# Optimization experiments

Measured on AMD Instinct MI355X. Metric: run time of the kernel, lower is better.

The kernel has to match this reference:

```python
import jax, jax.numpy as jnp
import numpy as np

NQ = 4  # n_qubits == hidden_dim, fixed by the hard-coded 4-wire encoder


def _cnot(state, c, t):
    # state: [B, 2,2,2,2]; wire w lives on axis w+1. Flip target where control==1.
    s = jnp.moveaxis(state, (c + 1, t + 1), (-2, -1))
    s = s.at[..., 1, :].set(s[..., 1, ::-1])
    return jnp.moveaxis(s, (-2, -1), (c + 1, t + 1))


def _qlayer(x, theta):
    """4-qubit circuit: RX(x_w) then RX(theta_w) on each wire (composed as one
    RX(x_w+theta_w) rotation, identical math), CNOT ring, PauliZ expectation.
    x: [B, 4] angles, theta: [4] trainable angles -> [B, 4] expectations."""
    half = (x + theta) * 0.5                      # [B,4]
    c = jnp.cos(half).astype(jnp.complex64)
    s = jnp.sin(half).astype(jnp.complex64)
    # RX(a)|0> = [cos(a/2), -i sin(a/2)]; product state of 4 qubits
    q = jnp.stack([c, -1j * s], axis=-1)          # [B,4,2]
    state = jnp.einsum('bi,bj,bk,bl->bijkl', q[:, 0], q[:, 1], q[:, 2], q[:, 3])
    # CNOT ring: (0,1), (1,2), (2,3), (3,0)
    state = _cnot(state, 0, 1)
    state = _cnot(state, 1, 2)
    state = _cnot(state, 2, 3)
    state = _cnot(state, 3, 0)
    p = jnp.real(state * jnp.conj(state))         # [B,2,2,2,2] probabilities
    sgn = jnp.asarray([1.0, -1.0], dtype=p.dtype)
    z0 = jnp.einsum('bijkl,i->b', p, sgn)
    z1 = jnp.einsum('bijkl,j->b', p, sgn)
    z2 = jnp.einsum('bijkl,k->b', p, sgn)
    z3 = jnp.einsum('bijkl,l->b', p, sgn)
    return jnp.stack([z0, z1, z2, z3], axis=-1)   # [B,4]


def setup_inputs() -> dict:
    key = jax.random.key(0)
    T, B, D, H = 512, 4096, 32, NQ
    ks = jax.random.split(key, 13)
    scale = 1.0 / np.sqrt(D + H)
    inp = {'inputs': jax.random.normal(ks[0], (T, B, D), dtype=jnp.float32)}
    names = ['f', 'i', 'u', 'o']
    for n, kw, kb, kt in zip(names, ks[1:5], ks[5:9], ks[9:13]):
        inp['W_' + n] = jax.random.uniform(kw, (D + H, NQ), jnp.float32, -scale, scale)
        inp['b_' + n] = jax.random.uniform(kb, (NQ,), jnp.float32, -scale, scale)
        inp['th_' + n] = jax.random.normal(kt, (NQ,), jnp.float32)
    return inp


def reference(inputs, W_f, b_f, W_i, b_i, W_u, b_u, W_o, b_o, th_f, th_i, th_u, th_o):
    B = inputs.shape[1]
    hx0 = jnp.zeros((B, NQ), dtype=inputs.dtype)
    cx0 = jnp.zeros((B, NQ), dtype=inputs.dtype)

    def step(carry, x):
        hx, cx = carry
        comb = jnp.concatenate([x, hx], axis=1)           # [B, D+H]
        f = jax.nn.sigmoid(_qlayer(comb @ W_f + b_f, th_f))
        i = jax.nn.sigmoid(_qlayer(comb @ W_i + b_i, th_i))
        g = jnp.tanh(_qlayer(comb @ W_u + b_u, th_u))
        o = jax.nn.sigmoid(_qlayer(comb @ W_o + b_o, th_o))
        cx2 = f * cx + i * g
        hx2 = o * jnp.tanh(cx2)
        return (hx2, cx2), hx2

    (hx, cx), outputs = jax.lax.scan(step, (hx0, cx0), inputs)
    return outputs, (hx, cx)
```

## Files before the change

### kernel.cpp

```cpp
#include <hip/hip_runtime.h>
#include <hip/hip_fp16.h>

#define TT 512
#define BB 4096
#define PD 16

__device__ __forceinline__ const float* sel4(int g, const float* a, const float* b,
                                             const float* c, const float* d) {
    return g == 0 ? a : (g == 1 ? b : (g == 2 ? c : d));
}

__device__ __forceinline__ float sigmoid_fast(float x) {
    float e = __expf(-x);
    return __builtin_amdgcn_rcpf(1.0f + e);
}
__device__ __forceinline__ float tanh_fast(float x) {
    float e = __expf(-2.0f * x);
    return fmaf(2.0f, __builtin_amdgcn_rcpf(1.0f + e), -1.0f);
}

template<int CTRL>
__device__ __forceinline__ float dppf(float v) {
    int i = __builtin_amdgcn_mov_dpp(__float_as_int(v), CTRL, 0xf, 0xf, true);
    return __int_as_float(i);
}
#define QP(a,b,c,d) ((a) | ((b) << 2) | ((c) << 4) | ((d) << 6))
template<int CTRL>
__device__ __forceinline__ float quad_bcast(float v) { return dppf<CTRL>(v); }

template<int OFS>
__device__ __forceinline__ float swzf(float v) {
    return __int_as_float(__builtin_amdgcn_ds_swizzle(__float_as_int(v), OFS));
}

__global__ __launch_bounds__(256) void qlstm_pre(
    const float* __restrict__ x,
    const float* __restrict__ Wf, const float* __restrict__ bf, const float* __restrict__ thf,
    const float* __restrict__ Wi, const float* __restrict__ bi, const float* __restrict__ thi,
    const float* __restrict__ Wu, const float* __restrict__ bu, const float* __restrict__ thu,
    const float* __restrict__ Wo, const float* __restrict__ bo, const float* __restrict__ tho,
    __half* __restrict__ Ax)
{
    __shared__ float4 Wl[32][4];
    __shared__ float4 bias4[4];
    __shared__ float xs[256 * 33];
    int tid = threadIdx.x;
    for (int idx = tid; idx < 512; idx += 256) {
        int j = idx >> 4, c = idx & 15, g = c >> 2, w = c & 3;
        ((float*)Wl)[idx] = sel4(g, Wf, Wi, Wu, Wo)[j * 4 + w];
    }
    if (tid < 16) {
        int g = tid >> 2, w = tid & 3;
        ((float*)bias4)[tid] = sel4(g, bf, bi, bu, bo)[w] + sel4(g, thf, thi, thu, tho)[w];
    }

    size_t rbase = (size_t)blockIdx.x * 256;
    const float4* xg = (const float4*)(x + rbase * 32);
#pragma unroll
    for (int it = 0; it < 8; ++it) {
        int i = it * 256 + tid;
        float4 v = xg[i];
        int r = i >> 3, c = (i & 7) * 4;
        float* p = &xs[r * 33 + c];
        p[0] = v.x; p[1] = v.y; p[2] = v.z; p[3] = v.w;
    }
    __syncthreads();

    float4 acc[4];
#pragma unroll
    for (int q = 0; q < 4; ++q) acc[q] = bias4[q];

    const float* xr = &xs[tid * 33];
#pragma unroll
    for (int j = 0; j < 32; ++j) {
        float xj = xr[j];
#pragma unroll
        for (int q = 0; q < 4; ++q) {
            float4 wv = Wl[j][q];
            acc[q].x = fmaf(xj, wv.x, acc[q].x);
            acc[q].y = fmaf(xj, wv.y, acc[q].y);
            acc[q].z = fmaf(xj, wv.z, acc[q].z);
            acc[q].w = fmaf(xj, wv.w, acc[q].w);
        }
    }

    union { __half2 h2; unsigned u; } cv;
    uint4 s0, s1;
    cv.h2 = __floats2half2_rn(acc[0].x, acc[0].y); s0.x = cv.u;
    cv.h2 = __floats2half2_rn(acc[0].z, acc[0].w); s0.y = cv.u;
    cv.h2 = __floats2half2_rn(acc[1].x, acc[1].y); s0.z = cv.u;
    cv.h2 = __floats2half2_rn(acc[1].z, acc[1].w); s0.w = cv.u;
    cv.h2 = __floats2half2_rn(acc[2].x, acc[2].y); s1.x = cv.u;
    cv.h2 = __floats2half2_rn(acc[2].z, acc[2].w); s1.y = cv.u;
    cv.h2 = __floats2half2_rn(acc[3].x, acc[3].y); s1.z = cv.u;
    cv.h2 = __floats2half2_rn(acc[3].z, acc[3].w); s1.w = cv.u;
    uint4* Ap = (uint4*)Ax + (rbase + tid) * 2;
    Ap[0] = s0; Ap[1] = s1;
}

__global__ __launch_bounds__(256) void qlstm_scan16(
    const __half* __restrict__ Ax,
    const float* __restrict__ Wf, const float* __restrict__ Wi,
    const float* __restrict__ Wu, const float* __restrict__ Wo,
    float* __restrict__ out)
{
    int tid = threadIdx.x;
    int gid = blockIdx.x * 256 + tid;
    int b   = gid >> 4;
    int L   = gid & 15;
    int w   = L & 3;
    int g   = L >> 2;

    const float* Wg = sel4(g, Wf, Wi, Wu, Wo);
    float whA = Wg[(32 + w) * 4 + w];
    float whB = Wg[(32 + (w ^ 1)) * 4 + w];
    float whC = Wg[(32 + (w ^ 2)) * 4 + w];
    float whD = Wg[(32 + (w ^ 3)) * 4 + w];
    bool isU = (g == 2);
    bool wb0 = (w & 1) != 0, wb1 = (w & 2) != 0;

    float d0 = isU ? 0.0f : 0.5f;
    float d1 = isU ? 1.0f : 0.25f;
    float d3 = isU ? -0.33333333f : -0.020833333f;
    float d5 = isU ? 0.13333333f : 0.0020833333f;
    float d7 = isU ? -0.03841007f : -0.000210846f;

    const __half* Axp = Ax + (size_t)b * 16 + L;
    float* outp4 = out + (size_t)b * 4 + L;

    float hx = 0.f, cx = 0.f;
    __half buf[PD];
#pragma unroll
    for (int k = 0; k < PD; ++k) buf[k] = Axp[(size_t)k * (BB * 16)];

#define SCAN_STEP(t, PREFETCH)                                                  \
    do {                                                                        \
        float ax = __half2float(buf[k]);                                        \
        if (PREFETCH) buf[k] = Axp[(size_t)((t) + PD) * (BB * 16)];             \
        float h1 = dppf<QP(1, 0, 3, 2)>(hx);                                    \
        float h2 = dppf<QP(2, 3, 0, 1)>(hx);                                    \
        float h3 = dppf<QP(3, 2, 1, 0)>(hx);                                    \
        float t1 = fmaf(hx, whA, ax);                                           \
        t1 = fmaf(h1, whB, t1);                                                 \
        float t2 = fmaf(h3, whD, h2 * whC);                                     \
        float C = __cosf(t1 + t2);                                              \
        float Cx1 = dppf<QP(1, 0, 3, 2)>(C);                                    \
        float P   = C * Cx1;                                                    \
        float Px2 = dppf<QP(2, 3, 0, 1)>(P);                                    \
        float Q   = P * Px2;                                                    \
        float m   = wb1 ? C : Cx1;                                              \
        float T   = Px2 * m;                                                    \
        float z   = wb0 ? (wb1 ? Q : P) : T;                                    \
        float z2  = z * z;                                                      \
        float pp  = fmaf(z2, d7, d5);                                           \
        pp = fmaf(z2, pp, d3);                                                  \
        pp = fmaf(z2, pp, d1);                                                  \
        float act = fmaf(z, pp, d0);                                            \
        float f = swzf<0x0013>(act);         \
        float i = swzf<0x0093>(act);                                \
        float u = swzf<0x0113>(act);                                \
        float o = swzf<0x0193>(act);                                \
        float c2 = fmaf(f, cx, i * u);                                          \
        cx = c2;                                                                \
        float q2 = c2 * c2;                                                     \
        float q4 = q2 * q2;                                                     \
        float dn = fmaf(q2, 420.0f, fmaf(q4, 15.0f, 945.0f));                   \
        float nm = c2 * fmaf(q2, 105.0f, 945.0f + q4);                          \
        hx = o * (nm * __builtin_amdgcn_rcpf(dn));                              \
        hxs[k] = hx;                                                            \
    } while (0)

    for (int tc = 0; tc < TT - PD; tc += PD) {
        float hxs[PD];
#pragma unroll
        for (int k = 0; k < PD; ++k) { int t = tc + k; SCAN_STEP(t, 1); }
        if (L < 4) {
#pragma unroll
            for (int k = 0; k < PD; ++k)
                outp4[(size_t)(tc + k) * 16384] = hxs[k];
        }
    }
    {
        float hxs[PD];
#pragma unroll
        for (int k = 0; k < PD; ++k) { int t = TT - PD + k; SCAN_STEP(t, 0); }
        if (L < 4) {
#pragma unroll
            for (int k = 0; k < PD; ++k)
                outp4[(size_t)(TT - PD + k) * 16384] = hxs[k];
        }
    }
    if (L < 4) {
        outp4[(size_t)TT * 16384] = hx;
        outp4[(size_t)TT * 16384 + 16384] = cx;
    }
#undef SCAN_STEP
}

__global__ __launch_bounds__(64, 1) void qlstm_scan_fb(
    const float* __restrict__ x,
    const float* __restrict__ Wf, const float* __restrict__ bf, const float* __restrict__ thf,
    const float* __restrict__ Wi, const float* __restrict__ bi, const float* __restrict__ thi,
    const float* __restrict__ Wu, const float* __restrict__ bu, const float* __restrict__ thu,
    const float* __restrict__ Wo, const float* __restrict__ bo, const float* __restrict__ tho,
    float* __restrict__ out)
{
    int lane = threadIdx.x;
    int gid  = blockIdx.x * 64 + lane;
    int b    = gid >> 2;
    int g    = lane & 3;

    const float* Wg = sel4(g, Wf, Wi, Wu, Wo);
    float wh[4][4];
#pragma unroll
    for (int j = 0; j < 4; ++j)
#pragma unroll
        for (int w = 0; w < 4; ++w)
            wh[j][w] = Wg[(32 + j) * 4 + w];

    __shared__ float4 Wl[32][4];
    float bias[4];
    for (int idx = lane; idx < 512; idx += 64) {
        int j = idx >> 4, c = idx & 15, gg = c >> 2, w = c & 3;
        ((float*)Wl)[idx] = sel4(gg, Wf, Wi, Wu, Wo)[j * 4 + w];
    }
#pragma unroll
    for (int w = 0; w < 4; ++w)
        bias[w] = sel4(g, bf, bi, bu, bo)[w] + sel4(g, thf, thi, thu, tho)[w];
    __syncthreads();

    float hx[4] = {0, 0, 0, 0}, cx[4] = {0, 0, 0, 0};
    const float4* xp = (const float4*)x + (size_t)b * 8;

    for (int t = 0; t < TT; ++t) {
        float4 xc[8];
#pragma unroll
        for (int k = 0; k < 8; ++k) xc[k] = xp[(size_t)t * (BB * 8) + k];
        float ax[4];
#pragma unroll
        for (int w = 0; w < 4; ++w) ax[w] = bias[w];
#pragma unroll
        for (int j = 0; j < 32; ++j) {
            float xj = ((const float*)xc)[j];
            float4 wv = Wl[j][g];
            ax[0] = fmaf(xj, wv.x, ax[0]);
            ax[1] = fmaf(xj, wv.y, ax[1]);
            ax[2] = fmaf(xj, wv.z, ax[2]);
            ax[3] = fmaf(xj, wv.w, ax[3]);
        }
        float C[4];
#pragma unroll
        for (int w = 0; w < 4; ++w) {
            float a0 = fmaf(hx[0], wh[0][w], ax[w]);
            float a1 = fmaf(hx[2], wh[2][w], hx[1] * wh[1][w]);
            a0 = fmaf(hx[3], wh[3][w], a0);
            C[w] = __cosf(a0 + a1);
        }
        float t12 = C[1] * C[2];
        float z[4];
        z[1] = C[0] * C[1];
        z[2] = C[0] * t12;
        z[0] = t12 * C[3];
        z[3] = z[2] * C[3];
        bool isU = (g == 2);
        float act[4];
#pragma unroll
        for (int w = 0; w < 4; ++w) {
            float zz = isU ? z[w] + z[w] : z[w];
            float y = sigmoid_fast(zz);
            act[w] = isU ? fmaf(2.0f, y, -1.0f) : y;
        }
#pragma unroll
        for (int w = 0; w < 4; ++w) {
            float fw = quad_bcast<QP(0, 0, 0, 0)>(act[w]);
            float iw = quad_bcast<QP(1, 1, 1, 1)>(act[w]);
            float uw = quad_bcast<QP(2, 2, 2, 2)>(act[w]);
            float ow = quad_bcast<QP(3, 3, 3, 3)>(act[w]);
            float c2 = fmaf(fw, cx[w], iw * uw);
            cx[w] = c2;
            hx[w] = ow * tanh_fast(c2);
        }
        float o01 = (g & 1) ? hx[1] : hx[0];
        float o23 = (g & 1) ? hx[3] : hx[2];
        out[(size_t)t * 16384 + gid] = (g & 2) ? o23 : o01;
    }
    float o01 = (g & 1) ? hx[1] : hx[0];
    float o23 = (g & 1) ? hx[3] : hx[2];
    out[(size_t)TT * 16384 + gid] = (g & 2) ? o23 : o01;
    float c01 = (g & 1) ? cx[1] : cx[0];
    float c23 = (g & 1) ? cx[3] : cx[2];
    out[(size_t)TT * 16384 + 16384 + gid] = (g & 2) ? c23 : c01;
}

extern "C" void kernel_launch(void* const* d_in, const int* in_sizes, int n_in,
                              void* d_out, int out_size, void* d_ws, size_t ws_size,
                              hipStream_t stream) {
    const float* x   = (const float*)d_in[0];
    const float* Wf  = (const float*)d_in[1];
    const float* bf  = (const float*)d_in[2];
    const float* thf = (const float*)d_in[3];
    const float* Wi  = (const float*)d_in[4];
    const float* bi  = (const float*)d_in[5];
    const float* thi = (const float*)d_in[6];
    const float* Wu  = (const float*)d_in[7];
    const float* bu  = (const float*)d_in[8];
    const float* thu = (const float*)d_in[9];
    const float* Wo  = (const float*)d_in[10];
    const float* bo  = (const float*)d_in[11];
    const float* tho = (const float*)d_in[12];
    float* out = (float*)d_out;

    size_t need = (size_t)TT * BB * 16 * sizeof(__half);
    if (ws_size >= need) {
        __half* Ax = (__half*)d_ws;
        qlstm_pre<<<(TT * BB) / 256, 256, 0, stream>>>(
            x, Wf, bf, thf, Wi, bi, thi, Wu, bu, thu, Wo, bo, tho, Ax);
        qlstm_scan16<<<(BB * 16) / 256, 256, 0, stream>>>(Ax, Wf, Wi, Wu, Wo, out);
    } else {
        qlstm_scan_fb<<<(BB * 4) / 64, 64, 0, stream>>>(
            x, Wf, bf, thf, Wi, bi, thi, Wu, bu, thu, Wo, bo, tho, out);
    }
}
```

Baseline: 128.9 us.

## Interleave two batch recurrences per thread in scan kernel with smaller blocks

Each thread now advances two independent batch rows' LSTM recurrences in lockstep, giving the serial per-step dependency chain instruction-level parallelism. Blocks shrink to 128 threads and the grid covers 16 rows per block, halving the total wave count. Prefetch depth drops to 8 per stream to keep register use in check. The trade-off is fewer waves per CU, which may leave SIMDs idle, in exchange for better latency hiding within each wave.

```diff
diff --git a/kernel.cpp b/kernel.cpp
--- a/kernel.cpp
+++ b/kernel.cpp
@@ -3,7 +3,7 @@
 
 #define TT 512
 #define BB 4096
-#define PD 16
+#define PD 8
 
 __device__ __forceinline__ const float* sel4(int g, const float* a, const float* b,
                                              const float* c, const float* d) {
@@ -98,18 +98,23 @@
     Ap[0] = s0; Ap[1] = s1;
 }
 
-__global__ __launch_bounds__(256) void qlstm_scan16(
+__global__ __launch_bounds__(128) void qlstm_scan2(
     const __half* __restrict__ Ax,
     const float* __restrict__ Wf, const float* __restrict__ Wi,
     const float* __restrict__ Wu, const float* __restrict__ Wo,
     float* __restrict__ out)
 {
-    int tid = threadIdx.x;
-    int gid = blockIdx.x * 256 + tid;
-    int b   = gid >> 4;
-    int L   = gid & 15;
-    int w   = L & 3;
-    int g   = L >> 2;
+    int tid  = threadIdx.x;
+    int lane = tid & 63;
+    int wv   = tid >> 6;
+    int grp  = lane >> 4;
+    int L    = lane & 15;
+    int w    = L & 3;
+    int g    = L >> 2;
+
+    int rbase = blockIdx.x * 16;
+    int rA = rbase + wv * 8 + grp;
+    int rB = rA + 4;
 
     const float* Wg = sel4(g, Wf, Wi, Wu, Wo);
     float whA = Wg[(32 + w) * 4 + w];
@@ -118,22 +123,26 @@
     float whD = Wg[(32 + (w ^ 3)) * 4 + w];
     bool isU = (g == 2);
     bool wb0 = (w & 1) != 0, wb1 = (w & 2) != 0;
-
     float d0 = isU ? 0.0f : 0.5f;
     float d1 = isU ? 1.0f : 0.25f;
     float d3 = isU ? -0.33333333f : -0.020833333f;
     float d5 = isU ? 0.13333333f : 0.0020833333f;
     float d7 = isU ? -0.03841007f : -0.000210846f;
 
-    const __half* Axp = Ax + (size_t)b * 16 + L;
-    float* outp4 = out + (size_t)b * 4 + L;
-
-    float hx = 0.f, cx = 0.f;
-    __half buf[PD];
-#pragma unroll
-    for (int k = 0; k < PD; ++k) buf[k] = Axp[(size_t)k * (BB * 16)];
-
-#define SCAN_STEP(t, PREFETCH)                                                  \
+    const __half* AxpA = Ax + (size_t)rA * 16 + L;
+    const __half* AxpB = Ax + (size_t)rB * 16 + L;
+    float* outA = out + (size_t)rA * 4 + L;
+    float* outB = out + (size_t)rB * 4 + L;
+
+    float hxA = 0.f, cxA = 0.f, hxB = 0.f, cxB = 0.f;
+    __half bufA[PD], bufB[PD];
+#pragma unroll
+    for (int k = 0; k < PD; ++k) {
+        bufA[k] = AxpA[(size_t)k * (BB * 16)];
+        bufB[k] = AxpB[(size_t)k * (BB * 16)];
+    }
+
+#define SCAN_STEP(hx, cx, buf, Axp, hxs, t, PREFETCH)                           \
     do {                                                                        \
         float ax = __half2float(buf[k]);                                        \
         if (PREFETCH) buf[k] = Axp[(size_t)((t) + PD) * (BB * 16)];             \
@@ -156,10 +165,10 @@
         pp = fmaf(z2, pp, d3);                                                  \
         pp = fmaf(z2, pp, d1);                                                  \
         float act = fmaf(z, pp, d0);                                            \
-        float f = swzf<0x0013>(act);         \
-        float i = swzf<0x0093>(act);                                \
-        float u = swzf<0x0113>(act);                                \
-        float o = swzf<0x0193>(act);                                \
+        float f = swzf<0x0013>(act);                                            \
+        float i = swzf<0x0093>(act);                                            \
+        float u = swzf<0x0113>(act);                                            \
+        float o = swzf<0x0193>(act);                                            \
         float c2 = fmaf(f, cx, i * u);                                          \
         cx = c2;                                                                \
         float q2 = c2 * c2;                                                     \
@@ -171,28 +180,42 @@
     } while (0)
 
     for (int tc = 0; tc < TT - PD; tc += PD) {
-        float hxs[PD];
-#pragma unroll
-        for (int k = 0; k < PD; ++k) { int t = tc + k; SCAN_STEP(t, 1); }
+        float hxsA[PD], hxsB[PD];
+#pragma unroll
+        for (int k = 0; k < PD; ++k) {
+            int t = tc + k;
+            SCAN_STEP(hxA, cxA, bufA, AxpA, hxsA, t, 1);
+            SCAN_STEP(hxB, cxB, bufB, AxpB, hxsB, t, 1);
+        }
         if (L < 4) {
 #pragma unroll
-            for (int k = 0; k < PD; ++k)
-                outp4[(size_t)(tc + k) * 16384] = hxs[k];
+            for (int k = 0; k < PD; ++k) {
+                outA[(size_t)(tc + k) * 16384] = hxsA[k];
+                outB[(size_t)(tc + k) * 16384] = hxsB[k];
+            }
         }
     }
     {
-        float hxs[PD];
-#pragma unroll
-        for (int k = 0; k < PD; ++k) { int t = TT - PD + k; SCAN_STEP(t, 0); }
+        float hxsA[PD], hxsB[PD];
+#pragma unroll
+        for (int k = 0; k < PD; ++k) {
+            int t = TT - PD + k;
+            SCAN_STEP(hxA, cxA, bufA, AxpA, hxsA, t, 0);
+            SCAN_STEP(hxB, cxB, bufB, AxpB, hxsB, t, 0);
+        }
         if (L < 4) {
 #pragma unroll
-            for (int k = 0; k < PD; ++k)
-                outp4[(size_t)(TT - PD + k) * 16384] = hxs[k];
+            for (int k = 0; k < PD; ++k) {
+                outA[(size_t)(TT - PD + k) * 16384] = hxsA[k];
+                outB[(size_t)(TT - PD + k) * 16384] = hxsB[k];
+            }
         }
     }
     if (L < 4) {
-        outp4[(size_t)TT * 16384] = hx;
-        outp4[(size_t)TT * 16384 + 16384] = cx;
+        outA[(size_t)TT * 16384] = hxA;
+        outA[(size_t)TT * 16384 + 16384] = cxA;
+        outB[(size_t)TT * 16384] = hxB;
+        outB[(size_t)TT * 16384 + 16384] = cxB;
     }
 #undef SCAN_STEP
 }
@@ -315,7 +338,7 @@
         __half* Ax = (__half*)d_ws;
         qlstm_pre<<<(TT * BB) / 256, 256, 0, stream>>>(
             x, Wf, bf, thf, Wi, bi, thi, Wu, bu, thu, Wo, bo, tho, Ax);
-        qlstm_scan16<<<(BB * 16) / 256, 256, 0, stream>>>(Ax, Wf, Wi, Wu, Wo, out);
+        qlstm_scan2<<<BB / 16, 128, 0, stream>>>(Ax, Wf, Wi, Wu, Wo, out);
     } else {
         qlstm_scan_fb<<<(BB * 4) / 64, 64, 0, stream>>>(
             x, Wf, bf, thf, Wi, bi, thi, Wu, bu, thu, Wo, bo, tho, out);
```

New measurement: 198.8 us. 1.54x slower.
